# Kernel tuning notes

Hardware: AMD Instinct MI355X
Metric: run time of the kernel (lower is better)

## Reference

```python
import jax, jax.numpy as jnp
import numpy as np
from math import pi

B, CIN, COUT, H, W, K, STRIDE, PAD = 4, 32, 64, 32, 32, 3, 1, 1


def setup_inputs() -> dict:
    key = jax.random.key(0)
    k1, k2, k3 = jax.random.split(key, 3)
    x = jax.random.normal(k1, (B, CIN, H, W), dtype=jnp.float32)
    probe = jax.random.uniform(k2, (1, CIN, COUT, 1, 1, K, K), dtype=jnp.float32, minval=-pi, maxval=pi)
    out_w = jax.random.uniform(k3, (1, CIN, COUT, 1, 1, K, K), dtype=jnp.float32, minval=-pi, maxval=pi)
    return {"x": x, "probe": probe, "out_w": out_w}


def _patches(x):
    # sliding-window gather, equivalent to x.unfold(2,K,S).unfold(3,K,S)
    p = jax.lax.conv_general_dilated_patches(
        x, filter_shape=(K, K), window_strides=(STRIDE, STRIDE),
        padding=[(PAD, PAD), (PAD, PAD)])  # (B, CIN*K*K, Ho, Wo), channel-major
    b, _, ho, wo = p.shape
    p = p.reshape(b, CIN, K, K, ho, wo)
    return jnp.transpose(p, (0, 1, 4, 5, 2, 3))  # (B, CIN, Ho, Wo, K, K)


def reference(x, probe, out_w):
    pat = _patches(x)[:, :, None]                 # (B, CIN, 1, Ho, Wo, K, K)
    act = jnp.cos(pat - probe) ** 3               # (B, CIN, COUT, Ho, Wo, K, K)
    cw = jnp.cos(out_w).reshape(CIN, COUT, K, K)  # squeeze broadcast dims
    sw = jnp.sin(out_w).reshape(CIN, COUT, K, K)
    out_x = jnp.einsum('cokl,bcohwkl->bohw', cw, act)
    out_y = jnp.einsum('cokl,bcohwkl->bohw', sw, act)
    return jnp.arctan2(out_y, out_x)              # (B, COUT, Ho, Wo)
```

## Files before the change

### kernel.cpp

```cpp
#include <hip/hip_runtime.h>
#include <math.h>

#define B_ 4
#define CIN_ 32
#define COUT_ 64
#define H_ 32
#define W_ 32

typedef _Float16 half8 __attribute__((ext_vector_type(8)));
typedef float floatx4 __attribute__((ext_vector_type(4)));

#define FEAT_BYTES (2u * 4 * 34 * 34 * 256)
#define NFEAT_THR (4 * 34 * 34 * 16)
#define NB_THR (9 * 128 * 16)

__global__ __launch_bounds__(256) void ring_prep(
    const float* __restrict__ x, const float* __restrict__ probe,
    const float* __restrict__ outw, char* __restrict__ ws) {
  int i = blockIdx.x * 256 + threadIdx.x;
  if (i < NFEAT_THR) {
    int p = i & 15;
    int t = i >> 4;
    int col = t % 34;
    t /= 34;
    int row = t % 34;
    int b = t / 34;
    int qd = p ^ (col & 7);
    int h = row - 1, w = col - 1;
    bool valid = (unsigned)h < 32u && (unsigned)w < 32u;
    half8 hi, lo;
#pragma unroll
    for (int half = 0; half < 2; ++half) {
      int c = qd * 2 + half;
      float c1 = 1.0f, s1 = 0.0f;
      if (valid) {
        float pv = x[((b * 32 + c) * 32 + h) * 32 + w];
        __sincosf(pv, &s1, &c1);
      }
      float c3 = c1 * fmaf(4.0f * c1, c1, -3.0f);
      float s3 = s1 * fmaf(-4.0f * s1, s1, 3.0f);
      float v4[4] = {c1, s1, c3, s3};
#pragma unroll
      for (int f = 0; f < 4; ++f) {
        _Float16 hv = (_Float16)v4[f];
        hi[half * 4 + f] = hv;
        lo[half * 4 + f] = (_Float16)((v4[f] - (float)hv) * 2048.0f);
      }
    }
    size_t off = (((size_t)(0 * 4 + b) * 34 + row) * 34 + col) * 256 + p * 16;
    size_t vstride = (size_t)4 * 34 * 34 * 256;
    *(half8*)(ws + off) = hi;
    *(half8*)(ws + off + vstride) = lo;
  } else if (i < NFEAT_THR + NB_THR) {
    int j = i - NFEAT_THR;
    int p = j & 15;
    int n = (j >> 4) & 127;
    int tap = j >> 11;
    int qd = p ^ (n & 7);
    int o = n & 63;
    int xy = n >> 6;
    half8 hi, lo;
#pragma unroll
    for (int half = 0; half < 2; ++half) {
      int c = qd * 2 + half;
      int idx = (c * 64 + o) * 9 + tap;
      float th = probe[idx];
      float wvv = outw[idx];
      float sth, cth, sw, cw;
      __sincosf(th, &sth, &cth);
      __sincosf(wvv, &sw, &cw);
      float c3 = cth * fmaf(4.0f * cth, cth, -3.0f);
      float s3 = sth * fmaf(-4.0f * sth, sth, 3.0f);
      float m = xy ? sw : cw;
      float v4[4] = {0.75f * m * cth, 0.75f * m * sth, 0.25f * m * c3,
                     0.25f * m * s3};
#pragma unroll
      for (int f = 0; f < 4; ++f) {
        _Float16 hv = (_Float16)v4[f];
        hi[half * 4 + f] = hv;
        lo[half * 4 + f] = (_Float16)((v4[f] - (float)hv) * 2048.0f);
      }
    }
    size_t off = FEAT_BYTES + (((size_t)(0 * 9 + tap) * 128 + n) * 256 + p * 16);
    size_t vstride = (size_t)9 * 128 * 256;
    *(half8*)(ws + off) = hi;
    *(half8*)(ws + off + vstride) = lo;
  }
}

__global__ __launch_bounds__(256, 2) void ring_mfma(
    const char* __restrict__ featg, const char* __restrict__ Bg,
    float* __restrict__ out) {
  __shared__ __align__(16) char sA[27648];
  __shared__ float sEx[512];

  int blk = blockIdx.x;
  int oh = blk & 1;
  int wt = (blk >> 1) & 1;
  int h = (blk >> 2) & 31;
  int b = blk >> 7;
  int tid = threadIdx.x;

  for (int u = tid; u < 1728; u += 256) {
    int v = u / 864;
    int r = (u - v * 864) / 288;
    int rest = u % 288;
    size_t goff = (size_t)v * (4u * 34 * 34 * 256) +
                  (((size_t)b * 34 + (h + r)) * 34 + wt * 16) * 256 + rest * 16;
    *(float4*)(sA + u * 16) = *(const float4*)(featg + goff);
  }

  int lane = tid & 63;
  int wv = tid >> 6;
  int n16 = lane & 15;
  int quad = lane >> 4;
  int xy = wv >> 1;
  int og = wv & 1;

  floatx4 acc0 = {0.f, 0.f, 0.f, 0.f};
  floatx4 acc1 = {0.f, 0.f, 0.f, 0.f};

  int n_global = xy * 64 + oh * 32 + og * 16 + n16;
  const char* bRow = Bg + (size_t)n_global * 256;
  int bkey = n16 & 7;

  __syncthreads();

#pragma unroll
  for (int tap = 0; tap < 9; ++tap) {
    int dk = tap / 3;
    int l = tap - dk * 3;
    int colidx = n16 + l;
    int akey = colidx & 7;
    const char* aH = sA + (dk * 18 + colidx) * 256;
    const char* aL = sA + ((3 + dk) * 18 + colidx) * 256;
    const char* bH = bRow + (size_t)tap * (128 * 256);
    const char* bL = bH + (size_t)9 * 128 * 256;

#pragma unroll
    for (int ks = 0; ks < 4; ++ks) {
      int q = ks * 4 + quad;
      int pa = (q ^ akey) * 16;
      int pb = (q ^ bkey) * 16;
      half8 Ah = *(const half8*)(aH + pa);
      half8 Al = *(const half8*)(aL + pa);
      half8 Bh = *(const half8*)(bH + pb);
      half8 Bl = *(const half8*)(bL + pb);
      acc0 = __builtin_amdgcn_mfma_f32_16x16x32_f16(Ah, Bh, acc0, 0, 0, 0);
      acc1 = __builtin_amdgcn_mfma_f32_16x16x32_f16(Al, Bh, acc1, 0, 0, 0);
      acc1 = __builtin_amdgcn_mfma_f32_16x16x32_f16(Ah, Bl, acc1, 0, 0, 0);
    }
  }

  floatx4 fin = acc0 + acc1 * (1.0f / 2048.0f);

  __syncthreads();
  if (xy == 1) {
#pragma unroll
    for (int r = 0; r < 4; ++r)
      sEx[(og * 16 + n16) * 16 + quad * 4 + r] = fin[r];
  }
  __syncthreads();
  if (xy == 0) {
    int o = oh * 32 + og * 16 + n16;
    float4 res;
    float* rp = (float*)&res;
#pragma unroll
    for (int r = 0; r < 4; ++r) {
      int m = quad * 4 + r;
      float ay = sEx[(og * 16 + n16) * 16 + m];
      rp[r] = atan2f(ay, fin[r]);
    }
    float* dst = out + (((size_t)(b * 64 + o) * 32 + h) * 32 + wt * 16 + quad * 4);
    *(float4*)dst = res;
  }
}

extern "C" void kernel_launch(void* const* d_in, const int* in_sizes, int n_in,
                              void* d_out, int out_size, void* d_ws, size_t ws_size,
                              hipStream_t stream) {
  const float* x = (const float*)d_in[0];
  const float* probe = (const float*)d_in[1];
  const float* outw = (const float*)d_in[2];
  char* ws = (char*)d_ws;
  float* out = (float*)d_out;

  int prep_threads = NFEAT_THR + NB_THR;
  ring_prep<<<(prep_threads + 255) / 256, 256, 0, stream>>>(x, probe, outw, ws);
  ring_mfma<<<512, 256, 0, stream>>>(ws, ws + FEAT_BYTES, out);
}
```

Baseline: 73.83 us.

## Compute input sin/cos features inside MFMA kernel instead of precomputing to workspace

```diff
diff --git a/kernel.cpp b/kernel.cpp
--- a/kernel.cpp
+++ b/kernel.cpp
@@ -1,95 +1,51 @@
 #include <hip/hip_runtime.h>
 #include <math.h>
 
-#define B_ 4
-#define CIN_ 32
-#define COUT_ 64
-#define H_ 32
-#define W_ 32
 
 typedef _Float16 half8 __attribute__((ext_vector_type(8)));
 typedef float floatx4 __attribute__((ext_vector_type(4)));
 
-#define FEAT_BYTES (2u * 4 * 34 * 34 * 256)
-#define NFEAT_THR (4 * 34 * 34 * 16)
-#define NB_THR (9 * 128 * 16)
+#define B_VSTRIDE (9u * 128 * 256)
 
-__global__ __launch_bounds__(256) void ring_prep(
-    const float* __restrict__ x, const float* __restrict__ probe,
-    const float* __restrict__ outw, char* __restrict__ ws) {
+__global__ __launch_bounds__(256) void ring_prep_b(
+    const float* __restrict__ probe, const float* __restrict__ outw,
+    char* __restrict__ Bg) {
   int i = blockIdx.x * 256 + threadIdx.x;
-  if (i < NFEAT_THR) {
-    int p = i & 15;
-    int t = i >> 4;
-    int col = t % 34;
-    t /= 34;
-    int row = t % 34;
-    int b = t / 34;
-    int qd = p ^ (col & 7);
-    int h = row - 1, w = col - 1;
-    bool valid = (unsigned)h < 32u && (unsigned)w < 32u;
-    half8 hi, lo;
+  int p = i & 15;
+  int n = (i >> 4) & 127;
+  int tap = i >> 11;
+  int qd = p ^ (n & 7);
+  int o = n & 63;
+  int xy = n >> 6;
+  half8 hi, lo;
 #pragma unroll
-    for (int half = 0; half < 2; ++half) {
-      int c = qd * 2 + half;
-      float c1 = 1.0f, s1 = 0.0f;
-      if (valid) {
-        float pv = x[((b * 32 + c) * 32 + h) * 32 + w];
-        __sincosf(pv, &s1, &c1);
-      }
-      float c3 = c1 * fmaf(4.0f * c1, c1, -3.0f);
-      float s3 = s1 * fmaf(-4.0f * s1, s1, 3.0f);
-      float v4[4] = {c1, s1, c3, s3};
+  for (int hf = 0; hf < 2; ++hf) {
+    int c = qd * 2 + hf;
+    int idx = (c * 64 + o) * 9 + tap;
+    float th = probe[idx];
+    float wvv = outw[idx];
+    float sth, cth, sw, cw;
+    __sincosf(th, &sth, &cth);
+    __sincosf(wvv, &sw, &cw);
+    float c3 = cth * fmaf(4.0f * cth, cth, -3.0f);
+    float s3 = sth * fmaf(-4.0f * sth, sth, 3.0f);
+    float m = xy ? sw : cw;
+    float v4[4] = {0.75f * m * cth, 0.75f * m * sth, 0.25f * m * c3,
+                   0.25f * m * s3};
 #pragma unroll
-      for (int f = 0; f < 4; ++f) {
-        _Float16 hv = (_Float16)v4[f];
-        hi[half * 4 + f] = hv;
-        lo[half * 4 + f] = (_Float16)((v4[f] - (float)hv) * 2048.0f);
-      }
+    for (int f = 0; f < 4; ++f) {
+      _Float16 hv = (_Float16)v4[f];
+      hi[hf * 4 + f] = hv;
+      lo[hf * 4 + f] = (_Float16)((v4[f] - (float)hv) * 2048.0f);
     }
-    size_t off = (((size_t)(0 * 4 + b) * 34 + row) * 34 + col) * 256 + p * 16;
-    size_t vstride = (size_t)4 * 34 * 34 * 256;
-    *(half8*)(ws + off) = hi;
-    *(half8*)(ws + off + vstride) = lo;
-  } else if (i < NFEAT_THR + NB_THR) {
-    int j = i - NFEAT_THR;
-    int p = j & 15;
-    int n = (j >> 4) & 127;
-    int tap = j >> 11;
-    int qd = p ^ (n & 7);
-    int o = n & 63;
-    int xy = n >> 6;
-    half8 hi, lo;
-#pragma unroll
-    for (int half = 0; half < 2; ++half) {
-      int c = qd * 2 + half;
-      int idx = (c * 64 + o) * 9 + tap;
-      float th = probe[idx];
-      float wvv = outw[idx];
-      float sth, cth, sw, cw;
-      __sincosf(th, &sth, &cth);
-      __sincosf(wvv, &sw, &cw);
-      float c3 = cth * fmaf(4.0f * cth, cth, -3.0f);
-      float s3 = sth * fmaf(-4.0f * sth, sth, 3.0f);
-      float m = xy ? sw : cw;
-      float v4[4] = {0.75f * m * cth, 0.75f * m * sth, 0.25f * m * c3,
-                     0.25f * m * s3};
-#pragma unroll
-      for (int f = 0; f < 4; ++f) {
-        _Float16 hv = (_Float16)v4[f];
-        hi[half * 4 + f] = hv;
-        lo[half * 4 + f] = (_Float16)((v4[f] - (float)hv) * 2048.0f);
-      }
-    }
-    size_t off = FEAT_BYTES + (((size_t)(0 * 9 + tap) * 128 + n) * 256 + p * 16);
-    size_t vstride = (size_t)9 * 128 * 256;
-    *(half8*)(ws + off) = hi;
-    *(half8*)(ws + off + vstride) = lo;
   }
+  size_t off = (((size_t)tap * 128 + n) * 16 + p) * 16;
+  *(half8*)(Bg + off) = hi;
+  *(half8*)(Bg + off + B_VSTRIDE) = lo;
 }
 
 __global__ __launch_bounds__(256, 2) void ring_mfma(
-    const char* __restrict__ featg, const char* __restrict__ Bg,
+    const float* __restrict__ x, const char* __restrict__ Bg,
     float* __restrict__ out) {
   __shared__ __align__(16) char sA[27648];
   __shared__ float sEx[512];
@@ -101,13 +57,36 @@
   int b = blk >> 7;
   int tid = threadIdx.x;
 
-  for (int u = tid; u < 1728; u += 256) {
-    int v = u / 864;
-    int r = (u - v * 864) / 288;
-    int rest = u % 288;
-    size_t goff = (size_t)v * (4u * 34 * 34 * 256) +
-                  (((size_t)b * 34 + (h + r)) * 34 + wt * 16) * 256 + rest * 16;
-    *(float4*)(sA + u * 16) = *(const float4*)(featg + goff);
+  for (int u = tid; u < 864; u += 256) {
+    int r = u / 288;
+    int t = u - r * 288;
+    int colidx = t >> 4;
+    int p = t & 15;
+    int q = p ^ (colidx & 7);
+    int hs = h + r - 1;
+    int wsx = wt * 16 + colidx - 1;
+    bool valid = ((unsigned)hs < 32u) && ((unsigned)wsx < 32u);
+    half8 hi, lo;
+#pragma unroll
+    for (int hf = 0; hf < 2; ++hf) {
+      int c = q * 2 + hf;
+      float c1 = 1.0f, s1 = 0.0f;
+      if (valid) {
+        float pv = x[((b * 32 + c) * 32 + hs) * 32 + wsx];
+        __sincosf(pv, &s1, &c1);
+      }
+      float c3 = c1 * fmaf(4.0f * c1, c1, -3.0f);
+      float s3 = s1 * fmaf(-4.0f * s1, s1, 3.0f);
+      float v4[4] = {c1, s1, c3, s3};
+#pragma unroll
+      for (int f = 0; f < 4; ++f) {
+        _Float16 hv = (_Float16)v4[f];
+        hi[hf * 4 + f] = hv;
+        lo[hf * 4 + f] = (_Float16)((v4[f] - (float)hv) * 2048.0f);
+      }
+    }
+    *(half8*)(sA + u * 16) = hi;
+    *(half8*)(sA + u * 16 + 13824) = lo;
   }
 
   int lane = tid & 63;
@@ -119,6 +98,7 @@
 
   floatx4 acc0 = {0.f, 0.f, 0.f, 0.f};
   floatx4 acc1 = {0.f, 0.f, 0.f, 0.f};
+  floatx4 acc2 = {0.f, 0.f, 0.f, 0.f};
 
   int n_global = xy * 64 + oh * 32 + og * 16 + n16;
   const char* bRow = Bg + (size_t)n_global * 256;
@@ -135,7 +115,7 @@
     const char* aH = sA + (dk * 18 + colidx) * 256;
     const char* aL = sA + ((3 + dk) * 18 + colidx) * 256;
     const char* bH = bRow + (size_t)tap * (128 * 256);
-    const char* bL = bH + (size_t)9 * 128 * 256;
+    const char* bL = bH + B_VSTRIDE;
 
 #pragma unroll
     for (int ks = 0; ks < 4; ++ks) {
@@ -148,11 +128,11 @@
       half8 Bl = *(const half8*)(bL + pb);
       acc0 = __builtin_amdgcn_mfma_f32_16x16x32_f16(Ah, Bh, acc0, 0, 0, 0);
       acc1 = __builtin_amdgcn_mfma_f32_16x16x32_f16(Al, Bh, acc1, 0, 0, 0);
-      acc1 = __builtin_amdgcn_mfma_f32_16x16x32_f16(Ah, Bl, acc1, 0, 0, 0);
+      acc2 = __builtin_amdgcn_mfma_f32_16x16x32_f16(Ah, Bl, acc2, 0, 0, 0);
     }
   }
 
-  floatx4 fin = acc0 + acc1 * (1.0f / 2048.0f);
+  floatx4 fin = acc0 + (acc1 + acc2) * (1.0f / 2048.0f);
 
   __syncthreads();
   if (xy == 1) {
@@ -182,10 +162,9 @@
   const float* x = (const float*)d_in[0];
   const float* probe = (const float*)d_in[1];
   const float* outw = (const float*)d_in[2];
-  char* ws = (char*)d_ws;
+  char* Bg = (char*)d_ws;
   float* out = (float*)d_out;
 
-  int prep_threads = NFEAT_THR + NB_THR;
-  ring_prep<<<(prep_threads + 255) / 256, 256, 0, stream>>>(x, probe, outw, ws);
-  ring_mfma<<<512, 256, 0, stream>>>(ws, ws + FEAT_BYTES, out);
+  ring_prep_b<<<72, 256, 0, stream>>>(probe, outw, Bg);
+  ring_mfma<<<512, 256, 0, stream>>>(x, Bg, out);
 }
```

New measurement: 71.21 us. 3.6% less time.
